# Kernel optimization log

Hardware: AMD Instinct MI355X
Metric: run time of the kernel (lower is better)

The kernel has to match this reference:

```python
import jax, jax.numpy as jnp
import numpy as np

N, C, H, W, K = 8, 512, 64, 64, 64
D = C // 4  # query/key dim


def setup_inputs() -> dict:
    key = jax.random.key(0)
    ks = jax.random.split(key, 17)
    s = 0.02
    return {
        "x1": jax.random.normal(ks[0], (N, C, H, W), jnp.float32),
        "y1": jax.random.normal(ks[1], (N, K, C), jnp.float32),
        "x2": jax.random.normal(ks[2], (N, C, H, W), jnp.float32),
        "y2": jax.random.normal(ks[3], (N, K, C), jnp.float32),
        "scale": jnp.zeros((1,), jnp.float32),
        "wq1": jax.random.normal(ks[4], (D, C), jnp.float32) * s,
        "bq1": jnp.zeros((D,), jnp.float32),
        "wk1": jax.random.normal(ks[5], (D, C), jnp.float32) * s,
        "bk1": jnp.zeros((D,), jnp.float32),
        "wv1": jax.random.normal(ks[6], (C, C), jnp.float32) * s,
        "bv1": jnp.zeros((C,), jnp.float32),
        "wq2": jax.random.normal(ks[7], (D, C), jnp.float32) * s,
        "bq2": jnp.zeros((D,), jnp.float32),
        "wk2": jax.random.normal(ks[8], (D, C), jnp.float32) * s,
        "bk2": jnp.zeros((C // 4,), jnp.float32),
        "wv2": jax.random.normal(ks[9], (C, C), jnp.float32) * s,
        "bv2": jnp.zeros((C,), jnp.float32),
    }


def reference(x1, y1, x2, y2, scale, wq1, bq1, wk1, bk1, wv1, bv1,
              wq2, bq2, wk2, bk2, wv2, bv2):
    n, c, h, w = x1.shape
    # 1x1 conv query: (N,C,H,W) -> (N, H*W, D)
    q1 = (jnp.einsum('nchw,dc->nhwd', x1, wq1) + bq1).reshape(n, h * w, -1)
    q2 = (jnp.einsum('nchw,dc->nhwd', x2, wq2) + bq2).reshape(n, h * w, -1)
    # linear key: (N,K,C) -> (N,K,D)
    k1 = y1 @ wk1.T + bk1
    k2 = y2 @ wk2.T + bk2
    # linear value: (N,K,C)
    v1 = y1 @ wv1.T + bv1
    v2 = y2 @ wv2.T + bv2
    # energies (N, HW, K), abs-diff fusion, softmax over centers K
    energy = jnp.abs(jnp.einsum('nld,nkd->nlk', q1, k1)
                     - jnp.einsum('nld,nkd->nlk', q2, k2))
    attn = jax.nn.softmax(energy, axis=-1)
    # weighted sums back to pixels: (N,C,HW) -> (N,C,H,W)
    out1 = jnp.einsum('nkc,nlk->ncl', v1, attn).reshape(n, c, h, w)
    out2 = jnp.einsum('nkc,nlk->ncl', v2, attn).reshape(n, c, h, w)
    out1 = scale[0] * out1 + x1
    out2 = scale[0] * out2 + x2
    return (out1, out2)
```

## Files before the change

### kernel.cpp

```cpp
#include <hip/hip_runtime.h>

#define NB 8
#define CC 512
#define HWL 4096
#define KK 64
#define DD 128

#define OFF_K1 0
#define OFF_K2 65536
#define OFF_V1 131072
#define OFF_V2 393216
#define OFF_AT 655360

__global__ __launch_bounds__(256) void kv_kernel(
    const float* __restrict__ scale,
    const float* __restrict__ y1, const float* __restrict__ y2,
    const float* __restrict__ wk1, const float* __restrict__ bk1,
    const float* __restrict__ wv1, const float* __restrict__ bv1,
    const float* __restrict__ wk2, const float* __restrict__ bk2,
    const float* __restrict__ wv2, const float* __restrict__ bv2,
    float* __restrict__ ws) {
  if (scale[0] == 0.0f) return;
  const int nk = blockIdx.x;
  const int n = nk / KK, k = nk % KK;
  __shared__ float sy1[CC], sy2[CC];
  for (int c = threadIdx.x; c < CC; c += blockDim.x) {
    sy1[c] = y1[(size_t)(n * KK + k) * CC + c];
    sy2[c] = y2[(size_t)(n * KK + k) * CC + c];
  }
  __syncthreads();
  float* K1 = ws + OFF_K1;
  float* K2 = ws + OFF_K2;
  float* V1 = ws + OFF_V1;
  float* V2 = ws + OFF_V2;
  for (int d = threadIdx.x; d < DD; d += blockDim.x) {
    float a1 = bk1[d], a2 = bk2[d];
    for (int c = 0; c < CC; ++c) {
      a1 += sy1[c] * wk1[(size_t)d * CC + c];
      a2 += sy2[c] * wk2[(size_t)d * CC + c];
    }
    K1[(size_t)(n * KK + k) * DD + d] = a1;
    K2[(size_t)(n * KK + k) * DD + d] = a2;
  }
  for (int co = threadIdx.x; co < CC; co += blockDim.x) {
    float a1 = bv1[co], a2 = bv2[co];
    for (int c = 0; c < CC; ++c) {
      a1 += sy1[c] * wv1[(size_t)co * CC + c];
      a2 += sy2[c] * wv2[(size_t)co * CC + c];
    }
    V1[(size_t)(n * KK + k) * CC + co] = a1;
    V2[(size_t)(n * KK + k) * CC + co] = a2;
  }
}

__global__ __launch_bounds__(128) void attn_kernel(
    const float* __restrict__ scale,
    const float* __restrict__ x1, const float* __restrict__ x2,
    const float* __restrict__ wq1, const float* __restrict__ bq1,
    const float* __restrict__ wq2, const float* __restrict__ bq2,
    const float* __restrict__ ws_in, float* __restrict__ ws_out) {
  if (scale[0] == 0.0f) return;
  __shared__ float sx1[CC], sx2[CC], sq1[DD], sq2[DD], se[KK];
  const float* K1 = ws_in + OFF_K1;
  const float* K2 = ws_in + OFF_K2;
  float* ATTN = ws_out + OFF_AT;
  const int d = threadIdx.x;

  for (int nl = blockIdx.x; nl < NB * HWL; nl += gridDim.x) {
    const int n = nl / HWL, l = nl % HWL;
    for (int c = threadIdx.x; c < CC; c += blockDim.x) {
      sx1[c] = x1[((size_t)n * CC + c) * HWL + l];
      sx2[c] = x2[((size_t)n * CC + c) * HWL + l];
    }
    __syncthreads();
    float a1 = bq1[d], a2 = bq2[d];
    for (int c = 0; c < CC; ++c) {
      a1 += sx1[c] * wq1[(size_t)d * CC + c];
      a2 += sx2[c] * wq2[(size_t)d * CC + c];
    }
    sq1[d] = a1;
    sq2[d] = a2;
    __syncthreads();
    if (threadIdx.x < KK) {
      const int k = threadIdx.x;
      const float* k1r = K1 + (size_t)(n * KK + k) * DD;
      const float* k2r = K2 + (size_t)(n * KK + k) * DD;
      float e1 = 0.f, e2 = 0.f;
      for (int dd = 0; dd < DD; ++dd) {
        e1 += sq1[dd] * k1r[dd];
        e2 += sq2[dd] * k2r[dd];
      }
      se[k] = fabsf(e1 - e2);
    }
    __syncthreads();
    if (threadIdx.x < KK) {
      const int k = threadIdx.x;
      float e = se[k];
      float m = e;
      for (int i = 1; i < KK; i <<= 1) m = fmaxf(m, __shfl_xor(m, i, 64));
      float ex = expf(e - m);
      float s = ex;
      for (int i = 1; i < KK; i <<= 1) s += __shfl_xor(s, i, 64);
      ATTN[((size_t)n * HWL + l) * KK + k] = ex / s;
    }
    __syncthreads();
  }
}

__global__ __launch_bounds__(256) void out_kernel(
    const float* __restrict__ scale,
    const float* __restrict__ x1, const float* __restrict__ x2,
    const float* __restrict__ ws, float* __restrict__ out) {
  const float s = scale[0];
  const size_t half = (size_t)NB * CC * HWL;
  const size_t tid = (size_t)blockIdx.x * blockDim.x + threadIdx.x;
  const size_t stride = (size_t)gridDim.x * blockDim.x;

  if (s == 0.0f) {
    const float4* src1 = (const float4*)x1;
    const float4* src2 = (const float4*)x2;
    float4* o = (float4*)out;
    const size_t half4 = half / 4;
    for (size_t i = tid; i < half4; i += stride) o[i] = src1[i];
    for (size_t i = tid; i < half4; i += stride) o[half4 + i] = src2[i];
    return;
  }

  const float* V1 = ws + OFF_V1;
  const float* V2 = ws + OFF_V2;
  const float* ATTN = ws + OFF_AT;
  for (size_t i = tid; i < half; i += stride) {
    const size_t n = i / ((size_t)CC * HWL);
    const size_t r = i % ((size_t)CC * HWL);
    const size_t c = r / HWL;
    const size_t l = r % HWL;
    const float* at = ATTN + (n * HWL + l) * KK;
    float a1 = 0.f, a2 = 0.f;
    for (int k = 0; k < KK; ++k) {
      a1 += at[k] * V1[(n * KK + k) * CC + c];
      a2 += at[k] * V2[(n * KK + k) * CC + c];
    }
    out[i] = s * a1 + x1[i];
    out[half + i] = s * a2 + x2[i];
  }
}

extern "C" void kernel_launch(void* const* d_in, const int* in_sizes, int n_in,
                              void* d_out, int out_size, void* d_ws, size_t ws_size,
                              hipStream_t stream) {
  const float* x1    = (const float*)d_in[0];
  const float* y1    = (const float*)d_in[1];
  const float* x2    = (const float*)d_in[2];
  const float* y2    = (const float*)d_in[3];
  const float* scale = (const float*)d_in[4];
  const float* wq1   = (const float*)d_in[5];
  const float* bq1   = (const float*)d_in[6];
  const float* wk1   = (const float*)d_in[7];
  const float* bk1   = (const float*)d_in[8];
  const float* wv1   = (const float*)d_in[9];
  const float* bv1   = (const float*)d_in[10];
  const float* wq2   = (const float*)d_in[11];
  const float* bq2   = (const float*)d_in[12];
  const float* wk2   = (const float*)d_in[13];
  const float* bk2   = (const float*)d_in[14];
  const float* wv2   = (const float*)d_in[15];
  const float* bv2   = (const float*)d_in[16];
  float* out = (float*)d_out;
  float* ws  = (float*)d_ws;

  hipLaunchKernelGGL(kv_kernel, dim3(NB * KK), dim3(256), 0, stream,
                     scale, y1, y2, wk1, bk1, wv1, bv1, wk2, bk2, wv2, bv2, ws);
  hipLaunchKernelGGL(attn_kernel, dim3(4096), dim3(128), 0, stream,
                     scale, x1, x2, wq1, bq1, wq2, bq2, ws, ws);
  hipLaunchKernelGGL(out_kernel, dim3(2048), dim3(256), 0, stream,
                     scale, x1, x2, ws, out);
}
```

Baseline: 52.45 us.

## Fuse attention and output kernels; use nontemporal stores in copy path

```diff
diff --git a/kernel.cpp b/kernel.cpp
--- a/kernel.cpp
+++ b/kernel.cpp
@@ -6,11 +6,12 @@
 #define KK 64
 #define DD 128
 
+typedef float floatx4 __attribute__((ext_vector_type(4)));
+
 #define OFF_K1 0
 #define OFF_K2 65536
 #define OFF_V1 131072
 #define OFF_V2 393216
-#define OFF_AT 655360
 
 __global__ __launch_bounds__(256) void kv_kernel(
     const float* __restrict__ scale,
@@ -53,18 +54,36 @@
   }
 }
 
-__global__ __launch_bounds__(128) void attn_kernel(
+__global__ __launch_bounds__(256) void attn_out_kernel(
     const float* __restrict__ scale,
     const float* __restrict__ x1, const float* __restrict__ x2,
     const float* __restrict__ wq1, const float* __restrict__ bq1,
     const float* __restrict__ wq2, const float* __restrict__ bq2,
-    const float* __restrict__ ws_in, float* __restrict__ ws_out) {
-  if (scale[0] == 0.0f) return;
-  __shared__ float sx1[CC], sx2[CC], sq1[DD], sq2[DD], se[KK];
-  const float* K1 = ws_in + OFF_K1;
-  const float* K2 = ws_in + OFF_K2;
-  float* ATTN = ws_out + OFF_AT;
-  const int d = threadIdx.x;
+    const float* __restrict__ ws, float* __restrict__ out) {
+  const float s = scale[0];
+  const size_t half = (size_t)NB * CC * HWL;
+
+  if (s == 0.0f) {
+    const floatx4* __restrict__ src1 = (const floatx4*)x1;
+    const floatx4* __restrict__ src2 = (const floatx4*)x2;
+    floatx4* __restrict__ o = (floatx4*)out;
+    const size_t half4 = half / 4;
+    const size_t tid = (size_t)blockIdx.x * blockDim.x + threadIdx.x;
+    const size_t stride = (size_t)gridDim.x * blockDim.x;
+    for (size_t i = tid; i < half4; i += stride) {
+      floatx4 a = src1[i];
+      floatx4 b = src2[i];
+      __builtin_nontemporal_store(a, o + i);
+      __builtin_nontemporal_store(b, o + half4 + i);
+    }
+    return;
+  }
+
+  __shared__ float sx1[CC], sx2[CC], sq1[DD], sq2[DD], sattn[KK];
+  const float* K1 = ws + OFF_K1;
+  const float* K2 = ws + OFF_K2;
+  const float* V1 = ws + OFF_V1;
+  const float* V2 = ws + OFF_V2;
 
   for (int nl = blockIdx.x; nl < NB * HWL; nl += gridDim.x) {
     const int n = nl / HWL, l = nl % HWL;
@@ -73,13 +92,16 @@
       sx2[c] = x2[((size_t)n * CC + c) * HWL + l];
     }
     __syncthreads();
-    float a1 = bq1[d], a2 = bq2[d];
-    for (int c = 0; c < CC; ++c) {
-      a1 += sx1[c] * wq1[(size_t)d * CC + c];
-      a2 += sx2[c] * wq2[(size_t)d * CC + c];
+    if (threadIdx.x < DD) {
+      const int d = threadIdx.x;
+      float a1 = bq1[d], a2 = bq2[d];
+      for (int c = 0; c < CC; ++c) {
+        a1 += sx1[c] * wq1[(size_t)d * CC + c];
+        a2 += sx2[c] * wq2[(size_t)d * CC + c];
+      }
+      sq1[d] = a1;
+      sq2[d] = a2;
     }
-    sq1[d] = a1;
-    sq2[d] = a2;
     __syncthreads();
     if (threadIdx.x < KK) {
       const int k = threadIdx.x;
@@ -90,58 +112,27 @@
         e1 += sq1[dd] * k1r[dd];
         e2 += sq2[dd] * k2r[dd];
       }
-      se[k] = fabsf(e1 - e2);
-    }
-    __syncthreads();
-    if (threadIdx.x < KK) {
-      const int k = threadIdx.x;
-      float e = se[k];
+      float e = fabsf(e1 - e2);
       float m = e;
       for (int i = 1; i < KK; i <<= 1) m = fmaxf(m, __shfl_xor(m, i, 64));
       float ex = expf(e - m);
-      float s = ex;
-      for (int i = 1; i < KK; i <<= 1) s += __shfl_xor(s, i, 64);
-      ATTN[((size_t)n * HWL + l) * KK + k] = ex / s;
+      float sm = ex;
+      for (int i = 1; i < KK; i <<= 1) sm += __shfl_xor(sm, i, 64);
+      sattn[k] = ex / sm;
     }
     __syncthreads();
-  }
-}
-
-__global__ __launch_bounds__(256) void out_kernel(
-    const float* __restrict__ scale,
-    const float* __restrict__ x1, const float* __restrict__ x2,
-    const float* __restrict__ ws, float* __restrict__ out) {
-  const float s = scale[0];
-  const size_t half = (size_t)NB * CC * HWL;
-  const size_t tid = (size_t)blockIdx.x * blockDim.x + threadIdx.x;
-  const size_t stride = (size_t)gridDim.x * blockDim.x;
-
-  if (s == 0.0f) {
-    const float4* src1 = (const float4*)x1;
-    const float4* src2 = (const float4*)x2;
-    float4* o = (float4*)out;
-    const size_t half4 = half / 4;
-    for (size_t i = tid; i < half4; i += stride) o[i] = src1[i];
-    for (size_t i = tid; i < half4; i += stride) o[half4 + i] = src2[i];
-    return;
-  }
-
-  const float* V1 = ws + OFF_V1;
-  const float* V2 = ws + OFF_V2;
-  const float* ATTN = ws + OFF_AT;
-  for (size_t i = tid; i < half; i += stride) {
-    const size_t n = i / ((size_t)CC * HWL);
-    const size_t r = i % ((size_t)CC * HWL);
-    const size_t c = r / HWL;
-    const size_t l = r % HWL;
-    const float* at = ATTN + (n * HWL + l) * KK;
-    float a1 = 0.f, a2 = 0.f;
-    for (int k = 0; k < KK; ++k) {
-      a1 += at[k] * V1[(n * KK + k) * CC + c];
-      a2 += at[k] * V2[(n * KK + k) * CC + c];
+    for (int c = threadIdx.x; c < CC; c += blockDim.x) {
+      float a1 = 0.f, a2 = 0.f;
+      for (int k = 0; k < KK; ++k) {
+        const float at = sattn[k];
+        a1 += at * V1[(size_t)(n * KK + k) * CC + c];
+        a2 += at * V2[(size_t)(n * KK + k) * CC + c];
+      }
+      const size_t idx = ((size_t)n * CC + c) * HWL + l;
+      out[idx] = s * a1 + sx1[c];
+      out[half + idx] = s * a2 + sx2[c];
     }
-    out[i] = s * a1 + x1[i];
-    out[half + i] = s * a2 + x2[i];
+    __syncthreads();
   }
 }
 
@@ -170,8 +161,6 @@
 
   hipLaunchKernelGGL(kv_kernel, dim3(NB * KK), dim3(256), 0, stream,
                      scale, y1, y2, wk1, bk1, wv1, bv1, wk2, bk2, wv2, bv2, ws);
-  hipLaunchKernelGGL(attn_kernel, dim3(4096), dim3(128), 0, stream,
-                     scale, x1, x2, wq1, bq1, wq2, bq2, ws, ws);
-  hipLaunchKernelGGL(out_kernel, dim3(2048), dim3(256), 0, stream,
-                     scale, x1, x2, ws, out);
+  hipLaunchKernelGGL(attn_out_kernel, dim3(2048), dim3(256), 0, stream,
+                     scale, x1, x2, wq1, bq1, wq2, bq2, ws, out);
 }
```

After: 51.05 us. -2.7%, faster.
